# Kernel optimization log

Measured on AMD Instinct MI355X. Metric: run time of the kernel, lower is better.

Reference implementation:

```python
import jax, jax.numpy as jnp
import numpy as np
import math

CHANNELS, BINS, HEADS, KSIZE = 4, 1024, 8, 3
ROT_DIM = BINS // HEADS // 2  # 64: rotate first half of each 128-dim head


def _rope(t):
    # t: [b, c, heads, w, d]; rotate first ROT_DIM dims, interleaved-pair style
    w = t.shape[-2]
    inv_freq = 1.0 / (10000.0 ** (jnp.arange(0, ROT_DIM, 2, dtype=jnp.float32) / ROT_DIM))
    freqs = jnp.arange(w, dtype=jnp.float32)[:, None] * inv_freq[None, :]   # [w, ROT_DIM//2]
    freqs = jnp.repeat(freqs, 2, axis=-1)                                    # [w, ROT_DIM]
    cos, sin = jnp.cos(freqs), jnp.sin(freqs)
    t_rot, t_pass = t[..., :ROT_DIM], t[..., ROT_DIM:]
    pair = t_rot.reshape(t_rot.shape[:-1] + (ROT_DIM // 2, 2))
    rotated = jnp.stack((-pair[..., 1], pair[..., 0]), axis=-1).reshape(t_rot.shape)
    return jnp.concatenate([t_rot * cos + rotated * sin, t_pass], axis=-1)


def _proj(x, w_lin, w_conv, b_conv):
    # MultichannelLinear: contract last dim with per-channel [out, in] weight
    y = jnp.einsum('bchi,coi->bcho', x, w_lin)
    # depthwise Conv2d, kernel (1, 3), padding (0, 1), groups = channels
    y = jax.lax.conv_general_dilated(
        y, w_conv, window_strides=(1, 1), padding=((0, 0), (1, 1)),
        dimension_numbers=('NCHW', 'OIHW', 'NCHW'), feature_group_count=CHANNELS)
    return y + b_conv[None, :, None, None]


def _split_heads(y):
    b, c, h, w = y.shape
    # transpose(2,3) -> [b,c,w,h]; reshape -> [b,c,w,heads,d]; permute -> [b,c,heads,w,d]
    return y.transpose(0, 1, 3, 2).reshape(b, c, w, HEADS, h // HEADS).transpose(0, 1, 3, 2, 4)


def setup_inputs() -> dict:
    key = jax.random.key(0)
    k1, k2, k3, k4, k5 = jax.random.split(key, 5)
    s_lin = 1.0 / math.sqrt(BINS)
    x = jax.random.normal(k1, (2, CHANNELS, BINS, BINS), dtype=jnp.float32)
    w_q_lin = jax.random.uniform(k2, (CHANNELS, BINS, BINS), jnp.float32, -s_lin, s_lin)
    w_q_conv = jax.random.uniform(k3, (CHANNELS, 1, 1, KSIZE), jnp.float32, -0.5, 0.5)
    b_q_conv = jax.random.uniform(k4, (CHANNELS,), jnp.float32, -0.5, 0.5)
    w_out = jax.random.uniform(k5, (CHANNELS, BINS, BINS), jnp.float32, -s_lin, s_lin)
    return {"x": x, "w_q_lin": w_q_lin, "w_q_conv": w_q_conv, "b_q_conv": b_q_conv, "w_out": w_out}


def reference(x, w_q_lin, w_q_conv, b_q_conv, w_out):
    b, c, h, w = x.shape
    # NOTE: original forward uses self.q_proj for q, k AND v (k_proj/v_proj unused)
    p = _proj(x, w_q_lin, w_q_conv, b_q_conv)          # [b,c,h,w]
    ph = _split_heads(p)                                # [b,c,heads,w,d]
    q = _rope(ph)
    k = _rope(ph)
    v = ph
    qk = jnp.einsum('bcnqd,bcnkd->bcnqk', q, k) / math.sqrt(h)
    a = jnp.einsum('bcnqk,bcnkd->bcnqd', jax.nn.softmax(qk, axis=-1), v)
    # merge heads back: [b,c,heads,w,d] -> [b,c,w,h] -> [b,c,h,w]
    a = a.transpose(0, 1, 3, 2, 4).reshape(b, c, w, h).transpose(0, 1, 3, 2)
    return jnp.einsum('bchi,coi->bcho', a, w_out)
```

## Files before the change

kernel.cpp:

```cpp
#include <hip/hip_runtime.h>
#include <cstdint>
#include <cstddef>

typedef __bf16 bf16;
typedef bf16 bf16x2 __attribute__((ext_vector_type(2)));
typedef bf16 bf16x4 __attribute__((ext_vector_type(4)));
typedef bf16 bf16x8 __attribute__((ext_vector_type(8)));
typedef float f32x4 __attribute__((ext_vector_type(4)));
typedef float f32x16 __attribute__((ext_vector_type(16)));

__device__ __forceinline__ void gload_lds16(const bf16* g, bf16* l) {
    __builtin_amdgcn_global_load_lds(
        (__attribute__((address_space(1))) void*)(uintptr_t)(g),
        (__attribute__((address_space(3))) void*)(l),
        16, 0, 0);
}

__global__ __launch_bounds__(256) void cvt3_kernel(const float* __restrict__ a,
                                                   bf16* __restrict__ oa, int na4,
                                                   const float* __restrict__ b,
                                                   bf16* __restrict__ ob, int nb4,
                                                   const float* __restrict__ c,
                                                   bf16* __restrict__ oc, int nc4) {
    int i = blockIdx.x * 256 + threadIdx.x;
    const float* in; bf16* out;
    if (i < na4) { in = a; out = oa; }
    else if (i < na4 + nb4) { in = b; out = ob; i -= na4; }
    else if (i < na4 + nb4 + nc4) { in = c; out = oc; i -= na4 + nb4; }
    else return;
    float4 v = ((const float4*)in)[i];
    bf16x4 o;
    o[0] = (bf16)v.x; o[1] = (bf16)v.y; o[2] = (bf16)v.z; o[3] = (bf16)v.w;
    *(bf16x4*)(out + (size_t)i * 4) = o;
}

__global__ __launch_bounds__(256) void rope_tab_kernel(float2* __restrict__ t) {
    int i = blockIdx.x * 256 + threadIdx.x;
    int w = i >> 5, j = i & 31;
    float inv = exp2f(-(float)j * (13.287712379549449f / 32.0f));
    float a = (float)w * inv;
    t[i] = make_float2(cosf(a), sinf(a));
}

template <bool F32OUT>
__global__ void __launch_bounds__(256) gemm_bt(const bf16* __restrict__ A,
                                               const bf16* __restrict__ B,
                                               void* __restrict__ Cout) {
    __shared__ alignas(16) bf16 As[128 * 64];
    __shared__ alignas(16) bf16 Bs[128 * 64];
    const int tid = threadIdx.x, lane = tid & 63, wave = tid >> 6;
    const int l15 = lane & 15, quad = lane >> 4;
    const int b = blockIdx.x;
    const int s = b & 7, mt = (b >> 3) & 7, nt = b >> 6;
    const bf16* Ab = A + ((size_t)s << 20) + (size_t)mt * 128 * 1024;
    const bf16* Bb = B + ((size_t)(s & 3) << 20) + (size_t)nt * 128 * 1024;
    const int wm = (wave >> 1) * 64, wn = (wave & 1) * 64;

    const f32x4 fzero = {0.f, 0.f, 0.f, 0.f};
    f32x4 acc[4][4];
    for (int i = 0; i < 4; ++i)
        for (int j = 0; j < 4; ++j) acc[i][j] = fzero;

    const int sr = wave * 8 + (lane >> 3);
    const int sc = (lane & 7) * 8;

    for (int kt = 0; kt < 16; ++kt) {
        __syncthreads();
        for (int it = 0; it < 4; ++it) {
            int r = it * 32 + sr;
            gload_lds16(Ab + (size_t)r * 1024 + kt * 64 + sc, As + r * 64 + sc);
            gload_lds16(Bb + (size_t)r * 1024 + kt * 64 + sc, Bs + r * 64 + sc);
        }
        __syncthreads();
        for (int kk = 0; kk < 2; ++kk) {
            bf16x8 af[4], bfr[4];
            for (int i = 0; i < 4; ++i)
                af[i] = *(const bf16x8*)(As + (wm + i * 16 + l15) * 64 + kk * 32 + quad * 8);
            for (int j = 0; j < 4; ++j)
                bfr[j] = *(const bf16x8*)(Bs + (wn + j * 16 + l15) * 64 + kk * 32 + quad * 8);
            for (int i = 0; i < 4; ++i)
                for (int j = 0; j < 4; ++j)
                    acc[i][j] = __builtin_amdgcn_mfma_f32_16x16x32_bf16(af[i], bfr[j],
                                                                        acc[i][j], 0, 0, 0);
        }
    }
    size_t cbase = ((size_t)s << 20) + (size_t)mt * 128 * 1024 + (size_t)nt * 128;
    for (int i = 0; i < 4; ++i)
        for (int j = 0; j < 4; ++j) {
            int m = wm + i * 16 + quad * 4;
            int n = wn + j * 16 + l15;
            for (int r = 0; r < 4; ++r) {
                float v = acc[i][j][r];
                if (F32OUT)
                    __builtin_nontemporal_store(
                        v, &((float*)Cout)[cbase + (size_t)(m + r) * 1024 + n]);
                else
                    __builtin_nontemporal_store(
                        (bf16)v, &((bf16*)Cout)[cbase + (size_t)(m + r) * 1024 + n]);
            }
        }
}

__global__ void __launch_bounds__(256) conv_rope_kernel(
    const bf16* __restrict__ Yb, const float* __restrict__ wconv,
    const float* __restrict__ bconv, bf16* __restrict__ Qhat,
    bf16* __restrict__ Vhat, const float2* __restrict__ rtab) {
    __shared__ float Pt[32][260];
    const int s = blockIdx.z, cch = s & 3;
    const int h0 = blockIdx.y * 32, w0 = blockIdx.x * 256;
    const bf16* Y = Yb + ((size_t)s << 20);
    const float k0 = wconv[cch * 3], k1 = wconv[cch * 3 + 1], k2 = wconv[cch * 3 + 2];
    const float bias = bconv[cch];
    const float SQS = 0.21233045f;
    const int head = h0 >> 7, dbase = h0 & 127;

    for (int it = 0; it < 4; ++it) {
        const int hh = threadIdx.x >> 3;
        const int wseg = (threadIdx.x & 7) + it * 8;
        const int h = h0 + hh, w = w0 + wseg * 8;
        const bf16* yrow = Y + ((size_t)h << 10);
        bf16x8 yv = *(const bf16x8*)(yrow + w);
        float yc[10];
        yc[0] = (w > 0) ? (float)yrow[w - 1] : 0.f;
        for (int i = 0; i < 8; ++i) yc[i + 1] = (float)yv[i];
        yc[9] = (w + 8 < 1024) ? (float)yrow[w + 8] : 0.f;
        for (int i = 0; i < 8; ++i) {
            float p = fmaf(k0, yc[i], fmaf(k1, yc[i + 1], fmaf(k2, yc[i + 2], bias)));
            Pt[hh][wseg * 8 + i] = p;
        }
    }
    __syncthreads();
    {
        const int g0 = blockIdx.x * 16;
        for (int it = 0; it < 4; ++it) {
            int idx = it * 256 + threadIdx.x;
            int vl = idx >> 5, dl = idx & 31;
            int gl = vl >> 1, hh = vl & 1;
            bf16x8 pv;
            for (int j = 0; j < 8; ++j) {
                int wl = gl * 16 + 4 * hh + (j & 3) + 8 * (j >> 2);
                pv[j] = (bf16)Pt[dl][wl];
            }
            *(bf16x8*)(Vhat + ((((size_t)s * 8 + head) * 128 + g0 * 2 + vl) << 10) +
                       (dbase + dl) * 8) = pv;
        }
    }
    {
        const int dcb = threadIdx.x >> 6;
        const int d0 = dbase + dcb * 8;
        const int hb0 = dcb * 8;
        for (int it = 0; it < 4; ++it) {
            const int wl = (threadIdx.x & 63) + it * 64;
            const int w = w0 + wl;
            float q[8];
            if (d0 < 64) {
                for (int j = 0; j < 8; j += 2) {
                    float2 cs = rtab[(w << 5) + ((d0 + j) >> 1)];
                    float a = Pt[hb0 + j][wl], b = Pt[hb0 + j + 1][wl];
                    q[j]     = fmaf(a, cs.x, -b * cs.y);
                    q[j + 1] = fmaf(b, cs.x,  a * cs.y);
                }
            } else {
                for (int j = 0; j < 8; ++j) q[j] = Pt[hb0 + j][wl];
            }
            bf16x8 qb;
            for (int j = 0; j < 8; ++j) qb[j] = (bf16)(q[j] * SQS);
            *(bf16x8*)(Qhat + ((((size_t)s * 8 + head) * 16 + (d0 >> 3)) << 13) +
                       (size_t)w * 8) = qb;
        }
    }
}

__global__ void __launch_bounds__(256, 2) attn_kernel(const bf16* __restrict__ Qhat,
                                                      const bf16* __restrict__ Vhat,
                                                      bf16* __restrict__ AO) {
    __shared__ alignas(16) char smem[66048];
    const int tid = threadIdx.x, lane = tid & 63, wave = tid >> 6;
    const int l31 = lane & 31, h = lane >> 5;
    const int b = blockIdx.x;
    const int sh = b & 63, qtile = b >> 6;
    const int s = sh >> 3, head = sh & 7, q0 = qtile * 128;
    const bf16* Qg = Qhat + (size_t)sh * 131072;
    const bf16* Vg = Vhat + (size_t)sh * 131072;

    const int myq = q0 + wave * 32 + l31;
    bf16x8 qf[8];
    for (int ks8 = 0; ks8 < 8; ++ks8)
        qf[ks8] = *(const bf16x8*)(Qg + (size_t)(ks8 * 2 + h) * 8192 + (size_t)myq * 8);

    f32x16 Oacc[4];
    for (int nt = 0; nt < 4; ++nt)
        for (int e = 0; e < 16; ++e) Oacc[nt][e] = 0.f;
    float lsum = 0.f;

    auto stage = [&](int kt, int buf) {
        bf16* Ks = (bf16*)(smem + buf * 32768);
        bf16* Vs = Ks + 8192;
        for (int t = 0; t < 4; ++t) {
            int dc = wave * 4 + t;
            gload_lds16(Qg + (size_t)dc * 8192 + (size_t)(kt * 64 + lane) * 8,
                        Ks + (dc * 64 + lane) * 8);
            int wc = dc >> 1, half = dc & 1;
            gload_lds16(Vg + (size_t)(kt * 8 + wc) * 1024 + (size_t)(half * 64 + lane) * 8,
                        Vs + (wc * 128 + half * 64 + lane) * 8);
        }
    };

    stage(0, 0);
    for (int kt = 0; kt < 16; ++kt) {
        __syncthreads();
        if (kt < 15) stage(kt + 1, (kt + 1) & 1);
        bf16* Ks = (bf16*)(smem + (kt & 1) * 32768);
        bf16* Vs = Ks + 8192;

        f32x16 st[2];
        for (int e = 0; e < 16; ++e) { st[0][e] = 0.f; st[1][e] = 0.f; }
        for (int ks8 = 0; ks8 < 8; ++ks8) {
            bf16x8 kf0 = *(const bf16x8*)(Ks + ((ks8 * 2 + h) * 64 + l31) * 8);
            bf16x8 kf1 = *(const bf16x8*)(Ks + ((ks8 * 2 + h) * 64 + 32 + l31) * 8);
            st[0] = __builtin_amdgcn_mfma_f32_32x32x16_bf16(kf0, qf[ks8], st[0], 0, 0, 0);
            st[1] = __builtin_amdgcn_mfma_f32_32x32x16_bf16(kf1, qf[ks8], st[1], 0, 0, 0);
        }

        bf16x8 pfr[4];
        float lacc = 0.f;
        for (int mt = 0; mt < 2; ++mt)
            for (int hh = 0; hh < 2; ++hh) {
                bf16x8 pf;
                for (int e = 0; e < 8; e += 2) {
                    float a = exp2f(st[mt][hh * 8 + e]);
                    float c = exp2f(st[mt][hh * 8 + e + 1]);
                    lacc += a + c;
                    pf[e] = (bf16)a;
                    pf[e + 1] = (bf16)c;
                }
                pfr[mt * 2 + hh] = pf;
            }
        lsum += lacc;

        for (int ks = 0; ks < 4; ++ks) {
            const bf16x8 pf = pfr[ks];
            for (int nt = 0; nt < 4; ++nt) {
                bf16x8 vf = *(const bf16x8*)(Vs + ((ks * 2 + h) * 128 + nt * 32 + l31) * 8);
                Oacc[nt] = __builtin_amdgcn_mfma_f32_32x32x16_bf16(pf, vf, Oacc[nt], 0, 0, 0);
            }
        }
    }

    lsum += __shfl_xor(lsum, 32);
    float* lsf = (float*)(smem + 65536) + wave * 32;
    if (lane < 32) lsf[lane] = 1.0f / lsum;
    f32x4 rv[4];
    __builtin_amdgcn_s_waitcnt(0);
    for (int rg = 0; rg < 4; ++rg)
        rv[rg] = *(const f32x4*)(lsf + 8 * rg + 4 * h);

    __syncthreads();
    bf16* Ot = (bf16*)smem;
    for (int nt = 0; nt < 4; ++nt) {
        int d = nt * 32 + l31;
        for (int rg = 0; rg < 4; ++rg) {
            int q = wave * 32 + 8 * rg + 4 * h;
            bf16x4 o4;
            for (int e = 0; e < 4; ++e)
                o4[e] = (bf16)(Oacc[nt][rg * 4 + e] * rv[rg][e]);
            *(bf16x4*)(Ot + d * 136 + q) = o4;
        }
    }
    __syncthreads();
    bf16* AOg = AO + ((size_t)s << 20);
    for (int it = 0; it < 8; ++it) {
        int d = it * 16 + (tid >> 4);
        int qc = (tid & 15) * 8;
        bf16x8 v = *(const bf16x8*)(Ot + d * 136 + qc);
        *(bf16x8*)(AOg + (size_t)(head * 128 + d) * 1024 + q0 + qc) = v;
    }
}

extern "C" void kernel_launch(void* const* d_in, const int* in_sizes, int n_in,
                              void* d_out, int out_size, void* d_ws, size_t ws_size,
                              hipStream_t stream) {
    const float* x  = (const float*)d_in[0];
    const float* wq = (const float*)d_in[1];
    const float* wc = (const float*)d_in[2];
    const float* bc = (const float*)d_in[3];
    const float* wo = (const float*)d_in[4];
    float* out = (float*)d_out;

    char* ws = (char*)d_ws;
    bf16* xb   = (bf16*)ws;
    bf16* wqb  = (bf16*)(ws + (16u << 20));
    bf16* wob  = (bf16*)(ws + (24u << 20));
    bf16* Yb   = (bf16*)(ws + (32u << 20));
    bf16* Qhat = (bf16*)(ws + (48u << 20));
    bf16* Vhat = (bf16*)(ws + (64u << 20));
    float2* rtab = (float2*)(ws + (80u << 20));
    bf16* AO   = xb;

    cvt3_kernel<<<16384, 256, 0, stream>>>(x, xb, 2097152, wq, wqb, 1048576,
                                           wo, wob, 1048576);
    rope_tab_kernel<<<128, 256, 0, stream>>>(rtab);

    gemm_bt<false><<<512, 256, 0, stream>>>(xb, wqb, Yb);
    conv_rope_kernel<<<dim3(4, 32, 8), 256, 0, stream>>>(Yb, wc, bc, Qhat, Vhat, rtab);
    attn_kernel<<<512, 256, 0, stream>>>(Qhat, Vhat, AO);
    gemm_bt<true><<<512, 256, 0, stream>>>(AO, wob, out);
}
```

Baseline: 227.2 us.

## Halve attention key tile to fit four blocks per CU; pad conv LDS; drop nontemporal stores

The attention kernel's key/value tile drops from 64 to 32 keys per step, so each double-buffered LDS stage shrinks and four blocks can share a CU instead of two, with twice as many loop iterations and barriers. The conv_rope shared tile row is padded from 260 to 261 floats to change its bank mapping. GEMM output stores switch from nontemporal to ordinary stores so the results stay cached for the next kernel. Risks include more sync overhead per key, less work per barrier, and register pressure under the tighter launch bound.

Measured after the change: 245.1 us. 1.08x slower.

```diff
diff --git a/kernel.cpp b/kernel.cpp
--- a/kernel.cpp
+++ b/kernel.cpp
@@ -92,11 +92,9 @@
             for (int r = 0; r < 4; ++r) {
                 float v = acc[i][j][r];
                 if (F32OUT)
-                    __builtin_nontemporal_store(
-                        v, &((float*)Cout)[cbase + (size_t)(m + r) * 1024 + n]);
+                    ((float*)Cout)[cbase + (size_t)(m + r) * 1024 + n] = v;
                 else
-                    __builtin_nontemporal_store(
-                        (bf16)v, &((bf16*)Cout)[cbase + (size_t)(m + r) * 1024 + n]);
+                    ((bf16*)Cout)[cbase + (size_t)(m + r) * 1024 + n] = (bf16)v;
             }
         }
 }
@@ -105,7 +103,7 @@
     const bf16* __restrict__ Yb, const float* __restrict__ wconv,
     const float* __restrict__ bconv, bf16* __restrict__ Qhat,
     bf16* __restrict__ Vhat, const float2* __restrict__ rtab) {
-    __shared__ float Pt[32][260];
+    __shared__ float Pt[32][261];
     const int s = blockIdx.z, cch = s & 3;
     const int h0 = blockIdx.y * 32, w0 = blockIdx.x * 256;
     const bf16* Y = Yb + ((size_t)s << 20);
@@ -171,10 +169,10 @@
     }
 }
 
-__global__ void __launch_bounds__(256, 2) attn_kernel(const bf16* __restrict__ Qhat,
+__global__ void __launch_bounds__(256, 4) attn_kernel(const bf16* __restrict__ Qhat,
                                                       const bf16* __restrict__ Vhat,
                                                       bf16* __restrict__ AO) {
-    __shared__ alignas(16) char smem[66048];
+    __shared__ alignas(16) char smem[35328];
     const int tid = threadIdx.x, lane = tid & 63, wave = tid >> 6;
     const int l31 = lane & 31, h = lane >> 5;
     const int b = blockIdx.x;
@@ -194,51 +192,48 @@
     float lsum = 0.f;
 
     auto stage = [&](int kt, int buf) {
-        bf16* Ks = (bf16*)(smem + buf * 32768);
-        bf16* Vs = Ks + 8192;
-        for (int t = 0; t < 4; ++t) {
-            int dc = wave * 4 + t;
-            gload_lds16(Qg + (size_t)dc * 8192 + (size_t)(kt * 64 + lane) * 8,
-                        Ks + (dc * 64 + lane) * 8);
-            int wc = dc >> 1, half = dc & 1;
-            gload_lds16(Vg + (size_t)(kt * 8 + wc) * 1024 + (size_t)(half * 64 + lane) * 8,
-                        Vs + (wc * 128 + half * 64 + lane) * 8);
+        bf16* Ks = (bf16*)(smem + buf * 16384);
+        bf16* Vs = Ks + 4096;
+        for (int t = 0; t < 2; ++t) {
+            int dc = wave * 4 + t * 2 + (lane >> 5);
+            gload_lds16(Qg + (size_t)dc * 8192 + (size_t)(kt * 32 + l31) * 8,
+                        Ks + (dc * 32 + l31) * 8);
+            int d = t * 64 + lane;
+            gload_lds16(Vg + (size_t)(kt * 4 + wave) * 1024 + (size_t)d * 8,
+                        Vs + (wave * 128 + d) * 8);
         }
     };
 
     stage(0, 0);
-    for (int kt = 0; kt < 16; ++kt) {
+    for (int kt = 0; kt < 32; ++kt) {
         __syncthreads();
-        if (kt < 15) stage(kt + 1, (kt + 1) & 1);
-        bf16* Ks = (bf16*)(smem + (kt & 1) * 32768);
-        bf16* Vs = Ks + 8192;
-
-        f32x16 st[2];
-        for (int e = 0; e < 16; ++e) { st[0][e] = 0.f; st[1][e] = 0.f; }
+        if (kt < 31) stage(kt + 1, (kt + 1) & 1);
+        bf16* Ks = (bf16*)(smem + (kt & 1) * 16384);
+        bf16* Vs = Ks + 4096;
+
+        f32x16 st;
+        for (int e = 0; e < 16; ++e) st[e] = 0.f;
         for (int ks8 = 0; ks8 < 8; ++ks8) {
-            bf16x8 kf0 = *(const bf16x8*)(Ks + ((ks8 * 2 + h) * 64 + l31) * 8);
-            bf16x8 kf1 = *(const bf16x8*)(Ks + ((ks8 * 2 + h) * 64 + 32 + l31) * 8);
-            st[0] = __builtin_amdgcn_mfma_f32_32x32x16_bf16(kf0, qf[ks8], st[0], 0, 0, 0);
-            st[1] = __builtin_amdgcn_mfma_f32_32x32x16_bf16(kf1, qf[ks8], st[1], 0, 0, 0);
-        }
-
-        bf16x8 pfr[4];
+            bf16x8 kf = *(const bf16x8*)(Ks + ((ks8 * 2 + h) * 32 + l31) * 8);
+            st = __builtin_amdgcn_mfma_f32_32x32x16_bf16(kf, qf[ks8], st, 0, 0, 0);
+        }
+
+        bf16x8 pfr[2];
         float lacc = 0.f;
-        for (int mt = 0; mt < 2; ++mt)
-            for (int hh = 0; hh < 2; ++hh) {
-                bf16x8 pf;
-                for (int e = 0; e < 8; e += 2) {
-                    float a = exp2f(st[mt][hh * 8 + e]);
-                    float c = exp2f(st[mt][hh * 8 + e + 1]);
-                    lacc += a + c;
-                    pf[e] = (bf16)a;
-                    pf[e + 1] = (bf16)c;
-                }
-                pfr[mt * 2 + hh] = pf;
-            }
+        for (int ks = 0; ks < 2; ++ks) {
+            bf16x8 pf;
+            for (int e = 0; e < 8; e += 2) {
+                float a = exp2f(st[ks * 8 + e]);
+                float c = exp2f(st[ks * 8 + e + 1]);
+                lacc += a + c;
+                pf[e] = (bf16)a;
+                pf[e + 1] = (bf16)c;
+            }
+            pfr[ks] = pf;
+        }
         lsum += lacc;
 
-        for (int ks = 0; ks < 4; ++ks) {
+        for (int ks = 0; ks < 2; ++ks) {
             const bf16x8 pf = pfr[ks];
             for (int nt = 0; nt < 4; ++nt) {
                 bf16x8 vf = *(const bf16x8*)(Vs + ((ks * 2 + h) * 128 + nt * 32 + l31) * 8);
@@ -248,7 +243,7 @@
     }
 
     lsum += __shfl_xor(lsum, 32);
-    float* lsf = (float*)(smem + 65536) + wave * 32;
+    float* lsf = (float*)(smem + 34816) + wave * 32;
     if (lane < 32) lsf[lane] = 1.0f / lsum;
     f32x4 rv[4];
     __builtin_amdgcn_s_waitcnt(0);
```
